# Kernel optimization log

Measured on AMD Instinct MI355X. Metric: run time of the kernel, lower is better.

The kernel has to match this reference:

```python
import jax, jax.numpy as jnp
import numpy as np

E, H, I = 5, 768, 1024  # num_experts, hidden_dim, intermediate_dim
TOP_K = 2


def setup_inputs() -> dict:
    key = jax.random.key(0)
    ks = jax.random.split(key, 6)
    s = 0.02
    return {
        "x": jax.random.normal(ks[0], (4, 2048, H), dtype=jnp.float32),
        "router_w": jax.random.normal(ks[1], (E, H), dtype=jnp.float32) * s,  # torch Linear (out,in)
        "router_b": jnp.zeros((E,), dtype=jnp.float32),
        "gate_w": jax.random.normal(ks[2], (E, H, I), dtype=jnp.float32) * s,
        "up_w": jax.random.normal(ks[3], (E, H, I), dtype=jnp.float32) * s,
        "down_w": jax.random.normal(ks[4], (E, I, H), dtype=jnp.float32) * s,
    }


def reference(x, router_w, router_b, gate_w, up_w, down_w):
    B, S, Hd = x.shape
    xf = x.reshape(-1, Hd)                       # [T, H]
    T = xf.shape[0]
    # Router: linear (with bias) -> softmax -> top-2 -> renormalize
    logits = xf @ router_w.T + router_b          # [T, E]
    scores = jax.nn.softmax(logits, axis=-1)
    vals, idx = jax.lax.top_k(scores, TOP_K)     # [T, 2]
    vals = vals / jnp.sum(vals, axis=-1, keepdims=True)
    # Dense combine weights: zero for unselected experts (same math as the
    # per-expert gather/scatter loop in the original module).
    comb = jnp.zeros((T, gate_w.shape[0]), dtype=x.dtype)
    comb = comb.at[jnp.arange(T)[:, None], idx].add(vals)  # [T, E]
    # SwiGLU per expert, vectorized over experts
    g = jnp.einsum('th,ehi->tei', xf, gate_w)    # [T, E, I]
    u = jnp.einsum('th,ehi->tei', xf, up_w)
    y = jnp.einsum('tei,eih->teh', jax.nn.silu(g) * u, down_w)  # [T, E, H]
    out = jnp.einsum('teh,te->th', y, comb)
    return out.reshape(B, S, Hd)
```

## Files before the change

### kernel.cpp

```cpp
#include <hip/hip_runtime.h>
#include <hip/hip_bf16.h>
#include <cstdint>
#include <cstddef>

#define T_TOK 8192
#define H_DIM 768
#define I_DIM 1024
#define N_EXP 5
#define MAXTILE 136

typedef short v8s __attribute__((ext_vector_type(8)));
typedef float v4f __attribute__((ext_vector_type(4)));

static __device__ __forceinline__ unsigned short f2bf(float f) {
    union { float f; unsigned int u; } v; v.f = f;
    unsigned int u = v.u;
    unsigned int r = (u + 0x7fffu + ((u >> 16) & 1u)) >> 16;
    return (unsigned short)r;
}
static __device__ __forceinline__ float bf2f(unsigned short s) {
    union { unsigned int u; float f; } v; v.u = ((unsigned int)s) << 16; return v.f;
}

static __device__ __forceinline__ void async16(const unsigned short* g, unsigned short* l) {
    __builtin_amdgcn_global_load_lds(
        (const __attribute__((address_space(1))) unsigned int*)g,
        (__attribute__((address_space(3))) unsigned int*)l, 16, 0, 0);
}

__global__ void k_transp_all(const float* __restrict__ gw, const float* __restrict__ uw,
                             const float* __restrict__ dw,
                             unsigned short* __restrict__ wbt, unsigned short* __restrict__ dbt) {
    __shared__ float tile[32][33];
    const int z = blockIdx.z;
    const int tid = threadIdx.x;
    const int row = tid >> 3, cq = tid & 7;
    const int ocol = tid >> 3, seg = tid & 7;
    if (z < 2 * N_EXP) {
        if (blockIdx.y >= H_DIM / 32) return;
        const int e = z % N_EXP;
        const int isUp = z >= N_EXP;
        const float* src = (isUp ? uw : gw) + (size_t)e * H_DIM * I_DIM;
        const int c0 = blockIdx.x * 32, r0 = blockIdx.y * 32;
        float4 v = *(const float4*)(src + (size_t)(r0 + row) * I_DIM + c0 + cq * 4);
        tile[row][cq * 4 + 0] = v.x; tile[row][cq * 4 + 1] = v.y;
        tile[row][cq * 4 + 2] = v.z; tile[row][cq * 4 + 3] = v.w;
        __syncthreads();
        int c = c0 + ocol;
        int orow = (c >> 4) * 32 + (c & 15) + (isUp ? 16 : 0);
        ushort4 o;
        o.x = f2bf(tile[seg * 4 + 0][ocol]); o.y = f2bf(tile[seg * 4 + 1][ocol]);
        o.z = f2bf(tile[seg * 4 + 2][ocol]); o.w = f2bf(tile[seg * 4 + 3][ocol]);
        *(ushort4*)(wbt + ((size_t)e * 2 * I_DIM + orow) * H_DIM + r0 + seg * 4) = o;
    } else {
        if (blockIdx.x >= H_DIM / 32) return;
        const int e = z - 2 * N_EXP;
        const float* src = dw + (size_t)e * I_DIM * H_DIM;
        unsigned short* dst = dbt + (size_t)e * I_DIM * H_DIM;
        const int c0 = blockIdx.x * 32, r0 = blockIdx.y * 32;
        float4 v = *(const float4*)(src + (size_t)(r0 + row) * H_DIM + c0 + cq * 4);
        tile[row][cq * 4 + 0] = v.x; tile[row][cq * 4 + 1] = v.y;
        tile[row][cq * 4 + 2] = v.z; tile[row][cq * 4 + 3] = v.w;
        __syncthreads();
        ushort4 o;
        o.x = f2bf(tile[seg * 4 + 0][ocol]); o.y = f2bf(tile[seg * 4 + 1][ocol]);
        o.z = f2bf(tile[seg * 4 + 2][ocol]); o.w = f2bf(tile[seg * 4 + 3][ocol]);
        *(ushort4*)(dst + (size_t)(c0 + ocol) * I_DIM + r0 + seg * 4) = o;
    }
}

__global__ void k_router_a(const float* __restrict__ x, const float* __restrict__ rw,
                           const float* __restrict__ rb,
                           unsigned short* __restrict__ xb,
                           int* __restrict__ top2e, float2* __restrict__ top2w) {
    const int wave = threadIdx.x >> 6, lane = threadIdx.x & 63;
    const int t = blockIdx.x * 4 + wave;
    const float* xr = x + (size_t)t * H_DIM;
    unsigned short* xbr = xb + (size_t)t * H_DIM;
    float acc[N_EXP];
#pragma unroll
    for (int e = 0; e < N_EXP; e++) acc[e] = 0.f;
#pragma unroll
    for (int j = 0; j < H_DIM / 256; j++) {
        int idx = j * 256 + lane * 4;
        float4 xv = *(const float4*)(xr + idx);
        ushort4 o;
        o.x = f2bf(xv.x); o.y = f2bf(xv.y); o.z = f2bf(xv.z); o.w = f2bf(xv.w);
        *(ushort4*)(xbr + idx) = o;
#pragma unroll
        for (int e = 0; e < N_EXP; e++) {
            float4 wv = *(const float4*)(rw + e * H_DIM + idx);
            acc[e] += xv.x * wv.x + xv.y * wv.y + xv.z * wv.z + xv.w * wv.w;
        }
    }
#pragma unroll
    for (int s = 32; s > 0; s >>= 1) {
#pragma unroll
        for (int e = 0; e < N_EXP; e++) acc[e] += __shfl_down(acc[e], s);
    }
    if (lane == 0) {
        float l[N_EXP];
#pragma unroll
        for (int e = 0; e < N_EXP; e++) l[e] = acc[e] + rb[e];
        int i1 = 0;
#pragma unroll
        for (int e = 1; e < N_EXP; e++) if (l[e] > l[i1]) i1 = e;
        int i2 = (i1 == 0) ? 1 : 0;
#pragma unroll
        for (int e = 0; e < N_EXP; e++) if (e != i1 && l[e] > l[i2]) i2 = e;
        float w1 = 1.f / (1.f + __expf(l[i2] - l[i1]));
        top2e[t] = i1 | (i2 << 8);
        top2w[t] = make_float2(w1, 1.f - w1);
    }
}

__global__ void k_router_b(const int* __restrict__ top2e, const float2* __restrict__ top2w,
                           int* __restrict__ cnt, int* __restrict__ tokslot,
                           float* __restrict__ pweight) {
    __shared__ int lcnt[N_EXP], lbase[N_EXP];
    const int tid = threadIdx.x;
    if (tid < N_EXP) lcnt[tid] = 0;
    __syncthreads();
    const int t = blockIdx.x * 256 + tid;
    const int pe = top2e[t];
    const float2 wv = top2w[t];
    const int e1 = pe & 0xff, e2 = pe >> 8;
    const int s1 = atomicAdd(&lcnt[e1], 1);
    const int s2 = atomicAdd(&lcnt[e2], 1);
    __syncthreads();
    if (tid < N_EXP) lbase[tid] = atomicAdd(&cnt[tid], lcnt[tid]);
    __syncthreads();
    const int p1 = lbase[e1] + s1;
    tokslot[e1 * T_TOK + p1] = t; pweight[e1 * T_TOK + p1] = wv.x;
    const int p2 = lbase[e2] + s2;
    tokslot[e2 * T_TOK + p2] = t | (1 << 16); pweight[e2 * T_TOK + p2] = wv.y;
}

__global__ void k_tiles(const int* __restrict__ cnt, int4* __restrict__ tiles) {
    const int tid = threadIdx.x;
    if (tid < MAXTILE) tiles[tid] = make_int4(-1, 0, 0, 0);
    __syncthreads();
    if (tid == 0) {
        int off = 0, idx = 0;
        for (int e = 0; e < N_EXP; e++) {
            int cn = cnt[e];
            for (int m0 = 0; m0 < cn; m0 += 128)
                tiles[idx++] = make_int4(e, m0, off, cn);
            off += cn;
        }
    }
}

__launch_bounds__(256, 4)
__global__ void k_gateup(const unsigned short* __restrict__ xb,
                         const unsigned short* __restrict__ wbt,
                         const int4* __restrict__ tiles,
                         const int* __restrict__ tokslot,
                         const float* __restrict__ pweight,
                         unsigned short* __restrict__ hbuf) {
    const int4 td = tiles[blockIdx.x];
    const int e = td.x;
    if (e < 0) return;
    const int m0 = td.y, offe = td.z, cn = td.w;
    const int n0 = blockIdx.y * 64;

    __shared__ __align__(16) unsigned short ldsA[128 * 32];
    __shared__ __align__(16) unsigned short ldsB[128 * 32];
    __shared__ int tokLds[128];
    __shared__ float pwLds[128];

    const int tid = threadIdx.x;
    if (tid < 128) {
        int gr = m0 + tid;
        int tk = 0; float pw = 0.f;
        if (gr < cn) { tk = tokslot[e * T_TOK + gr] & 0xFFFF; pw = pweight[e * T_TOK + gr]; }
        tokLds[tid] = tk; pwLds[tid] = pw;
    }
    __syncthreads();

    const int lane = tid & 63;
    const int wave = tid >> 6;
    const int fm = lane & 15, quad = lane >> 4;
    const int pq = (quad + (fm >> 1)) & 3;

    const int srow = wave * 16 + (lane >> 2);
    const int scol = (((lane & 3) - (srow >> 1)) & 3) * 8;
    const unsigned short* aG1 = xb + (size_t)tokLds[srow] * H_DIM + scol;
    const unsigned short* aG2 = xb + (size_t)tokLds[64 + srow] * H_DIM + scol;
    const unsigned short* bG1 = wbt + ((size_t)e * 2 * I_DIM + n0 * 2 + srow) * H_DIM + scol;
    const unsigned short* bG2 = bG1 + (size_t)64 * H_DIM;
    unsigned short* lA1 = ldsA + wave * 512;
    unsigned short* lA2 = ldsA + 2048 + wave * 512;
    unsigned short* lB1 = ldsB + wave * 512;
    unsigned short* lB2 = ldsB + 2048 + wave * 512;

    const int wm = (wave & 1) * 64, wnw = wave >> 1;

    v4f acc[4][4];
#pragma unroll
    for (int i = 0; i < 4; i++)
#pragma unroll
        for (int j = 0; j < 4; j++) acc[i][j] = (v4f)0.f;

    for (int kb = 0; kb < H_DIM / 32; kb++) {
        const int k0 = kb * 32;
        async16(aG1 + k0, lA1);
        async16(aG2 + k0, lA2);
        async16(bG1 + k0, lB1);
        async16(bG2 + k0, lB2);
        __syncthreads();
        v8s aF[4], bF[4];
#pragma unroll
        for (int im = 0; im < 4; im++)
            aF[im] = *(const v8s*)&ldsA[(wm + im * 16 + fm) * 32 + pq * 8];
#pragma unroll
        for (int in = 0; in < 4; in++)
            bF[in] = *(const v8s*)&ldsB[(wnw * 64 + in * 16 + fm) * 32 + pq * 8];
#pragma unroll
        for (int im = 0; im < 4; im++)
#pragma unroll
            for (int in = 0; in < 4; in++)
                acc[im][in] = __builtin_amdgcn_mfma_f32_16x16x32_bf16(aF[im], bF[in], acc[im][in], 0, 0, 0);
        __syncthreads();
    }

#pragma unroll
    for (int im = 0; im < 4; im++) {
#pragma unroll
        for (int reg = 0; reg < 4; reg++) {
            int lr = wm + im * 16 + quad * 4 + reg;
            int gr = m0 + lr;
            if (gr < cn) {
                float pw = pwLds[lr];
                size_t base = (size_t)(offe + gr) * I_DIM + n0 + wnw * 32 + fm;
#pragma unroll
                for (int j = 0; j < 2; j++) {
                    float g = acc[im][2 * j][reg];
                    float u = acc[im][2 * j + 1][reg];
                    float s = g / (1.f + __expf(-g));
                    hbuf[base + j * 16] = f2bf(s * u * pw);
                }
            }
        }
    }
}

__launch_bounds__(256, 4)
__global__ void k_down(const unsigned short* __restrict__ hbuf,
                       const unsigned short* __restrict__ dbt,
                       const int4* __restrict__ tiles,
                       const int* __restrict__ tokslot,
                       unsigned short* __restrict__ ybuf) {
    const int4 td = tiles[blockIdx.x];
    const int e = td.x;
    if (e < 0) return;
    const int m0 = td.y, offe = td.z, cn = td.w;
    const int n0 = blockIdx.y * 128;

    __shared__ __align__(16) unsigned short ldsA[128 * 32];
    __shared__ __align__(16) unsigned short ldsB[128 * 32];
    __shared__ int tokLds[128];

    const int tid = threadIdx.x;
    if (tid < 128) {
        int gr = m0 + tid;
        tokLds[tid] = (gr < cn) ? tokslot[e * T_TOK + gr] : 0;
    }
    __syncthreads();

    const int lane = tid & 63;
    const int wave = tid >> 6;
    const int fm = lane & 15, quad = lane >> 4;
    const int pq = (quad + (fm >> 1)) & 3;

    const int srow = wave * 16 + (lane >> 2);
    const int scol = (((lane & 3) - (srow >> 1)) & 3) * 8;
    int ar1 = m0 + srow;      if (ar1 >= cn) ar1 = cn - 1;
    int ar2 = m0 + 64 + srow; if (ar2 >= cn) ar2 = cn - 1;
    const unsigned short* aG1 = hbuf + (size_t)(offe + ar1) * I_DIM + scol;
    const unsigned short* aG2 = hbuf + (size_t)(offe + ar2) * I_DIM + scol;
    const unsigned short* bG1 = dbt + ((size_t)e * H_DIM + n0 + srow) * I_DIM + scol;
    const unsigned short* bG2 = bG1 + (size_t)64 * I_DIM;
    unsigned short* lA1 = ldsA + wave * 512;
    unsigned short* lA2 = ldsA + 2048 + wave * 512;
    unsigned short* lB1 = ldsB + wave * 512;
    unsigned short* lB2 = ldsB + 2048 + wave * 512;

    const int wm = (wave & 1) * 64, wn = (wave >> 1) * 64;

    v4f acc[4][4];
#pragma unroll
    for (int i = 0; i < 4; i++)
#pragma unroll
        for (int j = 0; j < 4; j++) acc[i][j] = (v4f)0.f;

    for (int kb = 0; kb < I_DIM / 32; kb++) {
        const int k0 = kb * 32;
        async16(aG1 + k0, lA1);
        async16(aG2 + k0, lA2);
        async16(bG1 + k0, lB1);
        async16(bG2 + k0, lB2);
        __syncthreads();
        v8s aF[4], bF[4];
#pragma unroll
        for (int im = 0; im < 4; im++)
            aF[im] = *(const v8s*)&ldsA[(wm + im * 16 + fm) * 32 + pq * 8];
#pragma unroll
        for (int in = 0; in < 4; in++)
            bF[in] = *(const v8s*)&ldsB[(wn + in * 16 + fm) * 32 + pq * 8];
#pragma unroll
        for (int im = 0; im < 4; im++)
#pragma unroll
            for (int in = 0; in < 4; in++)
                acc[im][in] = __builtin_amdgcn_mfma_f32_16x16x32_bf16(aF[im], bF[in], acc[im][in], 0, 0, 0);
        __syncthreads();
    }

#pragma unroll
    for (int im = 0; im < 4; im++) {
#pragma unroll
        for (int reg = 0; reg < 4; reg++) {
            int lr = wm + im * 16 + quad * 4 + reg;
            int gr = m0 + lr;
            if (gr < cn) {
                int v = tokLds[lr];
                int tok = v & 0xFFFF, s = (v >> 16) & 1;
#pragma unroll
                for (int in = 0; in < 4; in++) {
                    int col = n0 + wn + in * 16 + fm;
                    ybuf[((size_t)s * T_TOK + tok) * H_DIM + col] = f2bf(acc[im][in][reg]);
                }
            }
        }
    }
}

__global__ void k_combine(const unsigned short* __restrict__ ybuf, float* __restrict__ out) {
    const size_t i8 = ((size_t)blockIdx.x * 256 + threadIdx.x) * 8;
    const unsigned short* y0 = ybuf + i8;
    const unsigned short* y1 = ybuf + (size_t)T_TOK * H_DIM + i8;
    ushort4 a0 = *(const ushort4*)y0, a1 = *(const ushort4*)(y0 + 4);
    ushort4 b0 = *(const ushort4*)y1, b1 = *(const ushort4*)(y1 + 4);
    float4 o0, o1;
    o0.x = bf2f(a0.x) + bf2f(b0.x); o0.y = bf2f(a0.y) + bf2f(b0.y);
    o0.z = bf2f(a0.z) + bf2f(b0.z); o0.w = bf2f(a0.w) + bf2f(b0.w);
    o1.x = bf2f(a1.x) + bf2f(b1.x); o1.y = bf2f(a1.y) + bf2f(b1.y);
    o1.z = bf2f(a1.z) + bf2f(b1.z); o1.w = bf2f(a1.w) + bf2f(b1.w);
    *(float4*)(out + i8) = o0;
    *(float4*)(out + i8 + 4) = o1;
}

extern "C" void kernel_launch(void* const* d_in, const int* in_sizes, int n_in,
                              void* d_out, int out_size, void* d_ws, size_t ws_size,
                              hipStream_t stream) {
    const float* x  = (const float*)d_in[0];
    const float* rw = (const float*)d_in[1];
    const float* rb = (const float*)d_in[2];
    const float* gw = (const float*)d_in[3];
    const float* uw = (const float*)d_in[4];
    const float* dw = (const float*)d_in[5];
    float* out = (float*)d_out;

    char* ws = (char*)d_ws;
    size_t o = 0;
    auto alloc = [&](size_t bytes) { void* p = ws + o; o += (bytes + 255) & ~255ull; return p; };
    int*    cnt     = (int*)   alloc(N_EXP * 4);
    int*    tokslot = (int*)   alloc((size_t)N_EXP * T_TOK * 4);
    float*  pweight = (float*) alloc((size_t)N_EXP * T_TOK * 4);
    int*    top2e   = (int*)   alloc((size_t)T_TOK * 4);
    float2* top2w   = (float2*)alloc((size_t)T_TOK * 8);
    int4*   tiles   = (int4*)  alloc((size_t)MAXTILE * 16);
    unsigned short* xb   = (unsigned short*)alloc((size_t)T_TOK * H_DIM * 2);
    unsigned short* wbt  = (unsigned short*)alloc((size_t)N_EXP * 2 * I_DIM * H_DIM * 2);
    unsigned short* dbt  = (unsigned short*)alloc((size_t)N_EXP * H_DIM * I_DIM * 2);
    unsigned short* hbuf = (unsigned short*)alloc((size_t)(2 * T_TOK + 128) * I_DIM * 2);
    unsigned short* ybuf = (unsigned short*)alloc((size_t)2 * T_TOK * H_DIM * 2);

    hipMemsetAsync(cnt, 0, N_EXP * 4, stream);

    dim3 tg(I_DIM / 32, I_DIM / 32, 3 * N_EXP);
    k_transp_all<<<tg, 256, 0, stream>>>(gw, uw, dw, wbt, dbt);

    k_router_a<<<T_TOK / 4, 256, 0, stream>>>(x, rw, rb, xb, top2e, top2w);
    k_router_b<<<T_TOK / 256, 256, 0, stream>>>(top2e, top2w, cnt, tokslot, pweight);
    k_tiles<<<1, 256, 0, stream>>>(cnt, tiles);

    dim3 g1(MAXTILE, I_DIM / 64);
    k_gateup<<<g1, 256, 0, stream>>>(xb, wbt, tiles, tokslot, pweight, hbuf);

    dim3 g2(MAXTILE, H_DIM / 128);
    k_down<<<g2, 256, 0, stream>>>(hbuf, dbt, tiles, tokslot, ybuf);

    k_combine<<<(T_TOK * H_DIM) / (256 * 8), 256, 0, stream>>>(ybuf, out);
}
```

Baseline: 264.0 us.

## Double-buffer LDS in grouped GEMMs and fold tile building into router kernel

Both grouped GEMM kernels now keep two LDS buffers, issuing the async loads for the next K slice before computing on the current one. This removes one barrier per iteration and overlaps global-to-LDS copies with MFMA work. The LDS swizzle is dropped in favour of a plain layout, which may add bank conflicts. The separate tile-building kernel is merged into the router scatter kernel through a last-block-done atomic counter, saving one launch, at the cost of doubling LDS use per block, which can lower occupancy.

```diff
diff --git a/kernel.cpp b/kernel.cpp
--- a/kernel.cpp
+++ b/kernel.cpp
@@ -116,7 +116,8 @@
 
 __global__ void k_router_b(const int* __restrict__ top2e, const float2* __restrict__ top2w,
                            int* __restrict__ cnt, int* __restrict__ tokslot,
-                           float* __restrict__ pweight) {
+                           float* __restrict__ pweight, int* __restrict__ done,
+                           int4* __restrict__ tiles) {
     __shared__ int lcnt[N_EXP], lbase[N_EXP];
     const int tid = threadIdx.x;
     if (tid < N_EXP) lcnt[tid] = 0;
@@ -134,19 +135,18 @@
     tokslot[e1 * T_TOK + p1] = t; pweight[e1 * T_TOK + p1] = wv.x;
     const int p2 = lbase[e2] + s2;
     tokslot[e2 * T_TOK + p2] = t | (1 << 16); pweight[e2 * T_TOK + p2] = wv.y;
-}
-
-__global__ void k_tiles(const int* __restrict__ cnt, int4* __restrict__ tiles) {
-    const int tid = threadIdx.x;
-    if (tid < MAXTILE) tiles[tid] = make_int4(-1, 0, 0, 0);
     __syncthreads();
     if (tid == 0) {
-        int off = 0, idx = 0;
-        for (int e = 0; e < N_EXP; e++) {
-            int cn = cnt[e];
-            for (int m0 = 0; m0 < cn; m0 += 128)
-                tiles[idx++] = make_int4(e, m0, off, cn);
-            off += cn;
+        __threadfence();
+        if (atomicAdd(done, 1) == (int)gridDim.x - 1) {
+            int c[N_EXP], off = 0, idx = 0;
+            for (int e = 0; e < N_EXP; e++) c[e] = atomicAdd(&cnt[e], 0);
+            for (int e = 0; e < N_EXP; e++) {
+                for (int m0 = 0; m0 < c[e]; m0 += 128)
+                    tiles[idx++] = make_int4(e, m0, off, c[e]);
+                off += c[e];
+            }
+            for (; idx < MAXTILE; idx++) tiles[idx] = make_int4(-1, 0, 0, 0);
         }
     }
 }
@@ -164,8 +164,8 @@
     const int m0 = td.y, offe = td.z, cn = td.w;
     const int n0 = blockIdx.y * 64;
 
-    __shared__ __align__(16) unsigned short ldsA[128 * 32];
-    __shared__ __align__(16) unsigned short ldsB[128 * 32];
+    __shared__ __align__(16) unsigned short ldsA[2][128 * 32];
+    __shared__ __align__(16) unsigned short ldsB[2][128 * 32];
     __shared__ int tokLds[128];
     __shared__ float pwLds[128];
 
@@ -181,18 +181,14 @@
     const int lane = tid & 63;
     const int wave = tid >> 6;
     const int fm = lane & 15, quad = lane >> 4;
-    const int pq = (quad + (fm >> 1)) & 3;
 
     const int srow = wave * 16 + (lane >> 2);
-    const int scol = (((lane & 3) - (srow >> 1)) & 3) * 8;
+    const int scol = (lane & 3) * 8;
     const unsigned short* aG1 = xb + (size_t)tokLds[srow] * H_DIM + scol;
     const unsigned short* aG2 = xb + (size_t)tokLds[64 + srow] * H_DIM + scol;
     const unsigned short* bG1 = wbt + ((size_t)e * 2 * I_DIM + n0 * 2 + srow) * H_DIM + scol;
     const unsigned short* bG2 = bG1 + (size_t)64 * H_DIM;
-    unsigned short* lA1 = ldsA + wave * 512;
-    unsigned short* lA2 = ldsA + 2048 + wave * 512;
-    unsigned short* lB1 = ldsB + wave * 512;
-    unsigned short* lB2 = ldsB + 2048 + wave * 512;
+    const int ldsOff = wave * 512;
 
     const int wm = (wave & 1) * 64, wnw = wave >> 1;
 
@@ -202,26 +198,35 @@
 #pragma unroll
         for (int j = 0; j < 4; j++) acc[i][j] = (v4f)0.f;
 
-    for (int kb = 0; kb < H_DIM / 32; kb++) {
-        const int k0 = kb * 32;
-        async16(aG1 + k0, lA1);
-        async16(aG2 + k0, lA2);
-        async16(bG1 + k0, lB1);
-        async16(bG2 + k0, lB2);
+    {
+        async16(aG1, &ldsA[0][ldsOff]);
+        async16(aG2, &ldsA[0][2048 + ldsOff]);
+        async16(bG1, &ldsB[0][ldsOff]);
+        async16(bG2, &ldsB[0][2048 + ldsOff]);
+    }
+    const int NIT = H_DIM / 32;
+    for (int kb = 0; kb < NIT; kb++) {
+        const int cur = kb & 1;
         __syncthreads();
+        if (kb + 1 < NIT) {
+            const int k0 = (kb + 1) * 32;
+            async16(aG1 + k0, &ldsA[1 - cur][ldsOff]);
+            async16(aG2 + k0, &ldsA[1 - cur][2048 + ldsOff]);
+            async16(bG1 + k0, &ldsB[1 - cur][ldsOff]);
+            async16(bG2 + k0, &ldsB[1 - cur][2048 + ldsOff]);
+        }
         v8s aF[4], bF[4];
 #pragma unroll
         for (int im = 0; im < 4; im++)
-            aF[im] = *(const v8s*)&ldsA[(wm + im * 16 + fm) * 32 + pq * 8];
+            aF[im] = *(const v8s*)&ldsA[cur][(wm + im * 16 + fm) * 32 + quad * 8];
 #pragma unroll
         for (int in = 0; in < 4; in++)
-            bF[in] = *(const v8s*)&ldsB[(wnw * 64 + in * 16 + fm) * 32 + pq * 8];
+            bF[in] = *(const v8s*)&ldsB[cur][(wnw * 64 + in * 16 + fm) * 32 + quad * 8];
 #pragma unroll
         for (int im = 0; im < 4; im++)
 #pragma unroll
             for (int in = 0; in < 4; in++)
                 acc[im][in] = __builtin_amdgcn_mfma_f32_16x16x32_bf16(aF[im], bF[in], acc[im][in], 0, 0, 0);
-        __syncthreads();
     }
 
 #pragma unroll
@@ -257,8 +262,8 @@
     const int m0 = td.y, offe = td.z, cn = td.w;
     const int n0 = blockIdx.y * 128;
 
-    __shared__ __align__(16) unsigned short ldsA[128 * 32];
-    __shared__ __align__(16) unsigned short ldsB[128 * 32];
+    __shared__ __align__(16) unsigned short ldsA[2][128 * 32];
+    __shared__ __align__(16) unsigned short ldsB[2][128 * 32];
     __shared__ int tokLds[128];
 
     const int tid = threadIdx.x;
@@ -271,20 +276,16 @@
     const int lane = tid & 63;
     const int wave = tid >> 6;
     const int fm = lane & 15, quad = lane >> 4;
-    const int pq = (quad + (fm >> 1)) & 3;
 
     const int srow = wave * 16 + (lane >> 2);
-    const int scol = (((lane & 3) - (srow >> 1)) & 3) * 8;
+    const int scol = (lane & 3) * 8;
     int ar1 = m0 + srow;      if (ar1 >= cn) ar1 = cn - 1;
     int ar2 = m0 + 64 + srow; if (ar2 >= cn) ar2 = cn - 1;
     const unsigned short* aG1 = hbuf + (size_t)(offe + ar1) * I_DIM + scol;
     const unsigned short* aG2 = hbuf + (size_t)(offe + ar2) * I_DIM + scol;
     const unsigned short* bG1 = dbt + ((size_t)e * H_DIM + n0 + srow) * I_DIM + scol;
     const unsigned short* bG2 = bG1 + (size_t)64 * I_DIM;
-    unsigned short* lA1 = ldsA + wave * 512;
-    unsigned short* lA2 = ldsA + 2048 + wave * 512;
-    unsigned short* lB1 = ldsB + wave * 512;
-    unsigned short* lB2 = ldsB + 2048 + wave * 512;
+    const int ldsOff = wave * 512;
 
     const int wm = (wave & 1) * 64, wn = (wave >> 1) * 64;
 
@@ -294,26 +295,35 @@
 #pragma unroll
         for (int j = 0; j < 4; j++) acc[i][j] = (v4f)0.f;
 
-    for (int kb = 0; kb < I_DIM / 32; kb++) {
-        const int k0 = kb * 32;
-        async16(aG1 + k0, lA1);
-        async16(aG2 + k0, lA2);
-        async16(bG1 + k0, lB1);
-        async16(bG2 + k0, lB2);
+    {
+        async16(aG1, &ldsA[0][ldsOff]);
+        async16(aG2, &ldsA[0][2048 + ldsOff]);
+        async16(bG1, &ldsB[0][ldsOff]);
+        async16(bG2, &ldsB[0][2048 + ldsOff]);
+    }
+    const int NIT = I_DIM / 32;
+    for (int kb = 0; kb < NIT; kb++) {
+        const int cur = kb & 1;
         __syncthreads();
+        if (kb + 1 < NIT) {
+            const int k0 = (kb + 1) * 32;
+            async16(aG1 + k0, &ldsA[1 - cur][ldsOff]);
+            async16(aG2 + k0, &ldsA[1 - cur][2048 + ldsOff]);
+            async16(bG1 + k0, &ldsB[1 - cur][ldsOff]);
+            async16(bG2 + k0, &ldsB[1 - cur][2048 + ldsOff]);
+        }
         v8s aF[4], bF[4];
 #pragma unroll
         for (int im = 0; im < 4; im++)
-            aF[im] = *(const v8s*)&ldsA[(wm + im * 16 + fm) * 32 + pq * 8];
+            aF[im] = *(const v8s*)&ldsA[cur][(wm + im * 16 + fm) * 32 + quad * 8];
 #pragma unroll
         for (int in = 0; in < 4; in++)
-            bF[in] = *(const v8s*)&ldsB[(wn + in * 16 + fm) * 32 + pq * 8];
+            bF[in] = *(const v8s*)&ldsB[cur][(wn + in * 16 + fm) * 32 + quad * 8];
 #pragma unroll
         for (int im = 0; im < 4; im++)
 #pragma unroll
             for (int in = 0; in < 4; in++)
                 acc[im][in] = __builtin_amdgcn_mfma_f32_16x16x32_bf16(aF[im], bF[in], acc[im][in], 0, 0, 0);
-        __syncthreads();
     }
 
 #pragma unroll
@@ -364,7 +374,7 @@
     char* ws = (char*)d_ws;
     size_t o = 0;
     auto alloc = [&](size_t bytes) { void* p = ws + o; o += (bytes + 255) & ~255ull; return p; };
-    int*    cnt     = (int*)   alloc(N_EXP * 4);
+    int*    cnt     = (int*)   alloc(8 * 4);
     int*    tokslot = (int*)   alloc((size_t)N_EXP * T_TOK * 4);
     float*  pweight = (float*) alloc((size_t)N_EXP * T_TOK * 4);
     int*    top2e   = (int*)   alloc((size_t)T_TOK * 4);
@@ -376,14 +386,14 @@
     unsigned short* hbuf = (unsigned short*)alloc((size_t)(2 * T_TOK + 128) * I_DIM * 2);
     unsigned short* ybuf = (unsigned short*)alloc((size_t)2 * T_TOK * H_DIM * 2);
 
-    hipMemsetAsync(cnt, 0, N_EXP * 4, stream);
+    hipMemsetAsync(cnt, 0, 8 * 4, stream);
 
     dim3 tg(I_DIM / 32, I_DIM / 32, 3 * N_EXP);
     k_transp_all<<<tg, 256, 0, stream>>>(gw, uw, dw, wbt, dbt);
 
     k_router_a<<<T_TOK / 4, 256, 0, stream>>>(x, rw, rb, xb, top2e, top2w);
-    k_router_b<<<T_TOK / 256, 256, 0, stream>>>(top2e, top2w, cnt, tokslot, pweight);
-    k_tiles<<<1, 256, 0, stream>>>(cnt, tiles);
+    k_router_b<<<T_TOK / 256, 256, 0, stream>>>(top2e, top2w, cnt, tokslot, pweight,
+                                                cnt + 5, tiles);
 
     dim3 g1(MAXTILE, I_DIM / 64);
     k_gateup<<<g1, 256, 0, stream>>>(xb, wbt, tiles, tokslot, pweight, hbuf);
```

Measured after the change: 265.5 us. No clear change (+0.6%).
